# Performance work log

Hardware: AMD Instinct MI355X
Metric: run time of the kernel (lower is better)

Reference implementation:

```python
import jax, jax.numpy as jnp
import numpy as np
from jax import lax

B, CIN, COUT, H, W = 16, 128, 128, 128, 128
KH, KW = 3, 3
BLK_O, BLK_I = 32, 32          # block sizes over (out_ch, in_ch); kernel dims fully covered
PRUNING_RATE = 0.75


def _make_block_mask():
    # Reproduces blocksparse(): keep (1 - pruning_rate) of the channel blocks.
    nbo, nbi = COUT // BLK_O, CIN // BLK_I
    n_blocks = nbo * nbi
    n_keep = int(round(n_blocks * (1.0 - PRUNING_RATE)))
    rng = np.random.default_rng(42)
    keep = np.zeros(n_blocks, dtype=np.float32)
    keep[rng.permutation(n_blocks)[:n_keep]] = 1.0
    blk = keep.reshape(nbo, nbi)                     # [4, 4]
    m = np.kron(blk, np.ones((BLK_O, BLK_I), np.float32))   # [COUT, CIN]
    m = np.broadcast_to(m[:, :, None, None], (COUT, CIN, KH, KW))
    return jnp.asarray(np.ascontiguousarray(m))


def setup_inputs() -> dict:
    key = jax.random.key(0)
    k1, k2, k3 = jax.random.split(key, 3)
    x = jax.random.normal(k1, (B, CIN, H, W), dtype=jnp.float32)
    weight = jax.random.normal(k2, (COUT, CIN, KH, KW), dtype=jnp.float32) * 0.05
    bias = jax.random.normal(k3, (COUT,), dtype=jnp.float32) * 0.05
    mask = _make_block_mask()
    return {"x": x, "weight": weight, "bias": bias, "mask": mask}


def reference(x, weight, bias, mask):
    # weight = weight * mask, then standard dense conv2d (stride 1, pad 1, dil 1, groups 1)
    w = weight * mask
    y = lax.conv_general_dilated(
        x, w,
        window_strides=(1, 1),
        padding=((1, 1), (1, 1)),
        dimension_numbers=("NCHW", "OIHW", "NCHW"),
    )
    return y + bias[None, :, None, None]
```

## Files before the change

### kernel.cpp

```cpp
#include <hip/hip_runtime.h>

#define NBATCH 16
#define CIN_ 128
#define COUT_ 128
#define H_ 128
#define W_ 128
#define TH 4
#define NR (TH + 2)
#define PSTRIDE 32

typedef short bf16x8 __attribute__((ext_vector_type(8)));
typedef float f32x4 __attribute__((ext_vector_type(4)));
typedef unsigned short u16x8 __attribute__((ext_vector_type(8)));

__device__ __forceinline__ unsigned short f32_to_bf16(float f) {
  unsigned int u = __float_as_uint(f);
  u += 0x7fffu + ((u >> 16) & 1u);
  return (unsigned short)(u >> 16);
}

__global__ void make_lists_k(const float* __restrict__ mask, int* __restrict__ lists) {
  if (threadIdx.x == 0) {
    for (int i = 0; i < 20; ++i) lists[i] = 0;
    for (int ob = 0; ob < 4; ++ob) {
      int c = 0;
      for (int ib = 0; ib < 4; ++ib) {
        float v = mask[(size_t)((ob * 32) * CIN_ + ib * 32) * 9];
        if (v != 0.0f) { lists[4 + ob * 4 + c] = ib; ++c; }
      }
      lists[ob] = c;
    }
  }
}

__global__ __launch_bounds__(256) void pack_w_k(const float* __restrict__ weight,
                                                const float* __restrict__ mask,
                                                const int* __restrict__ lists,
                                                unsigned short* __restrict__ wpack) {
  const int khkw = blockIdx.x;
  const int slot = blockIdx.y;
  const int ob   = blockIdx.z;
  if (slot >= lists[ob]) return;
  const int ib = lists[4 + ob * 4 + slot];
  const int kh = khkw / 3, kw = khkw % 3;
  for (int e = threadIdx.x; e < 1024; e += 256) {
    const int co = e >> 5, ci = e & 31;
    const int cog = ob * 32 + co, cig = ib * 32 + ci;
    const size_t widx = ((size_t)(cog * CIN_ + cig) * 3 + kh) * 3 + kw;
    const float v = weight[widx] * mask[widx];
    wpack[(size_t)((ob * 4 + slot) * 9 + khkw) * 1024 + e] = f32_to_bf16(v);
  }
}

__global__ __launch_bounds__(256, 3) void conv_fused_k(const float* __restrict__ x,
                                                       const unsigned short* __restrict__ wpack,
                                                       const int* __restrict__ lists,
                                                       const float* __restrict__ bias,
                                                       float* __restrict__ out) {
  __shared__ unsigned short xs[NR * 130 * PSTRIDE];

  const int tid  = threadIdx.x;
  const int wave = tid >> 6;
  const int lane = tid & 63;
  const int wl   = lane & 15;
  const int kg   = lane >> 4;

  const int h0 = blockIdx.x * TH;
  const int b  = blockIdx.y;
  const int ob = blockIdx.z;
  const int w0 = wave * 32;

  const int cnt = lists[ob];

  f32x4 acc[TH][2][2] = {};

  const int g   = tid & 7;
  const int q   = tid >> 3;
  const int oct = g & 3;

  for (int s = 0; s < cnt; ++s) {
    const int ib = lists[4 + ob * 4 + s];

    if (s) __syncthreads();

    {
      const float* xbase =
          x + ((size_t)b * CIN_ + ib * 32 + oct * 8) * H_ * W_ + q * 4;
#pragma unroll
      for (int it = 0; it < 3; ++it) {
        const int r = it * 2 + (g >> 2);
        const int row = h0 - 1 + r;
        const bool rv = (row >= 0) && (row < H_);
        const float* src = xbase + (size_t)(rv ? row : 0) * W_;
        f32x4 v0 = *(const f32x4*)(src);
        f32x4 v1 = *(const f32x4*)(src + 1 * (size_t)H_ * W_);
        f32x4 v2 = *(const f32x4*)(src + 2 * (size_t)H_ * W_);
        f32x4 v3 = *(const f32x4*)(src + 3 * (size_t)H_ * W_);
        f32x4 v4 = *(const f32x4*)(src + 4 * (size_t)H_ * W_);
        f32x4 v5 = *(const f32x4*)(src + 5 * (size_t)H_ * W_);
        f32x4 v6 = *(const f32x4*)(src + 6 * (size_t)H_ * W_);
        f32x4 v7 = *(const f32x4*)(src + 7 * (size_t)H_ * W_);
#pragma unroll
        for (int j = 0; j < 4; ++j) {
          u16x8 o;
          if (rv) {
            o[0] = f32_to_bf16(v0[j]); o[1] = f32_to_bf16(v1[j]);
            o[2] = f32_to_bf16(v2[j]); o[3] = f32_to_bf16(v3[j]);
            o[4] = f32_to_bf16(v4[j]); o[5] = f32_to_bf16(v5[j]);
            o[6] = f32_to_bf16(v6[j]); o[7] = f32_to_bf16(v7[j]);
          } else {
            o = u16x8{0, 0, 0, 0, 0, 0, 0, 0};
          }
          *(u16x8*)(xs + (r * 130 + q * 4 + 1 + j) * PSTRIDE + oct * 8) = o;
        }
      }
      for (int e = tid; e < NR * 2 * 32; e += 256) {
        const int r = e >> 6, edge = (e >> 5) & 1, cc = e & 31;
        xs[(r * 130 + (edge ? 129 : 0)) * PSTRIDE + cc] = 0;
      }
    }

    const unsigned short* wk =
        wpack + (size_t)((ob * 4 + s) * 9) * 1024 + wl * 32 + kg * 8;
    bf16x8 a[3][3][2];
#pragma unroll
    for (int kh = 0; kh < 3; ++kh)
#pragma unroll
      for (int kw = 0; kw < 3; ++kw) {
        a[kh][kw][0] = *(const bf16x8*)(wk + (kh * 3 + kw) * 1024);
        a[kh][kw][1] = *(const bf16x8*)(wk + (kh * 3 + kw) * 1024 + 16 * 32);
      }

    __syncthreads();

#pragma unroll
    for (int ridx = 0; ridx < NR; ++ridx) {
      bf16x8 bf[2][3];
#pragma unroll
      for (int ni = 0; ni < 2; ++ni)
#pragma unroll
        for (int kw = 0; kw < 3; ++kw)
          bf[ni][kw] = *(const bf16x8*)(xs + (ridx * 130 + w0 + ni * 16 + wl + kw) * PSTRIDE + kg * 8);

#pragma unroll
      for (int kh = 0; kh < 3; ++kh) {
        const int hi = ridx - kh;
        if (hi < 0 || hi >= TH) continue;
#pragma unroll
        for (int kw = 0; kw < 3; ++kw) {
          acc[hi][0][0] = __builtin_amdgcn_mfma_f32_16x16x32_bf16(a[kh][kw][0], bf[0][kw], acc[hi][0][0], 0, 0, 0);
          acc[hi][0][1] = __builtin_amdgcn_mfma_f32_16x16x32_bf16(a[kh][kw][0], bf[1][kw], acc[hi][0][1], 0, 0, 0);
          acc[hi][1][0] = __builtin_amdgcn_mfma_f32_16x16x32_bf16(a[kh][kw][1], bf[0][kw], acc[hi][1][0], 0, 0, 0);
          acc[hi][1][1] = __builtin_amdgcn_mfma_f32_16x16x32_bf16(a[kh][kw][1], bf[1][kw], acc[hi][1][1], 0, 0, 0);
        }
      }
    }
  }

#pragma unroll
  for (int mi = 0; mi < 2; ++mi)
#pragma unroll
    for (int j = 0; j < 4; ++j) {
      const int co = mi * 16 + kg * 4 + j;
      const float bv = bias[ob * 32 + co];
#pragma unroll
      for (int hh = 0; hh < TH; ++hh) {
        float* yrow = out + ((size_t)(b * COUT_ + ob * 32 + co) * H_ + h0 + hh) * W_;
        yrow[w0 + wl]      = acc[hh][mi][0][j] + bv;
        yrow[w0 + wl + 16] = acc[hh][mi][1][j] + bv;
      }
    }
}

extern "C" void kernel_launch(void* const* d_in, const int* in_sizes, int n_in,
                              void* d_out, int out_size, void* d_ws, size_t ws_size,
                              hipStream_t stream) {
  const float* x      = (const float*)d_in[0];
  const float* weight = (const float*)d_in[1];
  const float* bias   = (const float*)d_in[2];
  const float* mask   = (const float*)d_in[3];
  float* out = (float*)d_out;

  int* lists = (int*)d_ws;
  unsigned short* wpack = (unsigned short*)((char*)d_ws + 4096);

  make_lists_k<<<1, 64, 0, stream>>>(mask, lists);
  pack_w_k<<<dim3(9, 4, 4), 256, 0, stream>>>(weight, mask, lists, wpack);
  conv_fused_k<<<dim3(H_ / TH, NBATCH, 4), 256, 0, stream>>>(x, wpack, lists, bias, out);
}
```

Measured before the change: 79.63 us.

## Drop list kernel, swizzle LDS input tile, stage output through LDS for vector stores

Removes the single-thread list-building kernel and instead has each block derive the kept input-channel blocks from the mask with a wave ballot and bit tricks, saving one launch. Applies an XOR swizzle to the LDS pixel layout to reduce bank conflicts on the MFMA operand reads. Rewrites the epilogue to stage accumulators through LDS so each lane writes contiguous 16-byte float4 stores instead of scattered scalar stores, adding a barrier and extra LDS traffic.

```diff
diff --git a/kernel.cpp b/kernel.cpp
--- a/kernel.cpp
+++ b/kernel.cpp
@@ -19,29 +19,27 @@
   return (unsigned short)(u >> 16);
 }
 
-__global__ void make_lists_k(const float* __restrict__ mask, int* __restrict__ lists) {
-  if (threadIdx.x == 0) {
-    for (int i = 0; i < 20; ++i) lists[i] = 0;
-    for (int ob = 0; ob < 4; ++ob) {
-      int c = 0;
-      for (int ib = 0; ib < 4; ++ib) {
-        float v = mask[(size_t)((ob * 32) * CIN_ + ib * 32) * 9];
-        if (v != 0.0f) { lists[4 + ob * 4 + c] = ib; ++c; }
-      }
-      lists[ob] = c;
-    }
-  }
+__device__ __forceinline__ int lx(int pix, int hw) {
+  return (pix * PSTRIDE + hw) ^ (((pix >> 2) & 1) << 5);
+}
+
+__device__ __forceinline__ int mask_bits(const float* __restrict__ mask, int ob, int lane) {
+  float mv = (lane < 4) ? mask[((size_t)(ob * 32) * CIN_ + lane * 32) * 9] : 0.0f;
+  unsigned long long bal = __ballot(mv != 0.0f);
+  return (int)(bal & 15ull);
 }
 
 __global__ __launch_bounds__(256) void pack_w_k(const float* __restrict__ weight,
                                                 const float* __restrict__ mask,
-                                                const int* __restrict__ lists,
                                                 unsigned short* __restrict__ wpack) {
   const int khkw = blockIdx.x;
   const int slot = blockIdx.y;
   const int ob   = blockIdx.z;
-  if (slot >= lists[ob]) return;
-  const int ib = lists[4 + ob * 4 + slot];
+  const int mb = mask_bits(mask, ob, threadIdx.x & 63);
+  if (slot >= __popc(mb)) return;
+  int m = mb;
+  for (int t = 0; t < slot; ++t) m &= m - 1;
+  const int ib = __ffs(m) - 1;
   const int kh = khkw / 3, kw = khkw % 3;
   for (int e = threadIdx.x; e < 1024; e += 256) {
     const int co = e >> 5, ci = e & 31;
@@ -54,10 +52,10 @@
 
 __global__ __launch_bounds__(256, 3) void conv_fused_k(const float* __restrict__ x,
                                                        const unsigned short* __restrict__ wpack,
-                                                       const int* __restrict__ lists,
+                                                       const float* __restrict__ mask,
                                                        const float* __restrict__ bias,
                                                        float* __restrict__ out) {
-  __shared__ unsigned short xs[NR * 130 * PSTRIDE];
+  __shared__ __align__(16) unsigned short xs[NR * 130 * PSTRIDE];
 
   const int tid  = threadIdx.x;
   const int wave = tid >> 6;
@@ -70,7 +68,8 @@
   const int ob = blockIdx.z;
   const int w0 = wave * 32;
 
-  const int cnt = lists[ob];
+  const int mb  = mask_bits(mask, ob, lane);
+  const int cnt = __popc(mb);
 
   f32x4 acc[TH][2][2] = {};
 
@@ -78,8 +77,10 @@
   const int q   = tid >> 3;
   const int oct = g & 3;
 
+  int mrem = mb;
   for (int s = 0; s < cnt; ++s) {
-    const int ib = lists[4 + ob * 4 + s];
+    const int ib = __ffs(mrem) - 1;
+    mrem &= mrem - 1;
 
     if (s) __syncthreads();
 
@@ -111,12 +112,12 @@
           } else {
             o = u16x8{0, 0, 0, 0, 0, 0, 0, 0};
           }
-          *(u16x8*)(xs + (r * 130 + q * 4 + 1 + j) * PSTRIDE + oct * 8) = o;
+          *(u16x8*)(xs + lx(r * 130 + q * 4 + 1 + j, oct * 8)) = o;
         }
       }
       for (int e = tid; e < NR * 2 * 32; e += 256) {
         const int r = e >> 6, edge = (e >> 5) & 1, cc = e & 31;
-        xs[(r * 130 + (edge ? 129 : 0)) * PSTRIDE + cc] = 0;
+        xs[lx(r * 130 + (edge ? 129 : 0), cc)] = 0;
       }
     }
 
@@ -140,7 +141,7 @@
       for (int ni = 0; ni < 2; ++ni)
 #pragma unroll
         for (int kw = 0; kw < 3; ++kw)
-          bf[ni][kw] = *(const bf16x8*)(xs + (ridx * 130 + w0 + ni * 16 + wl + kw) * PSTRIDE + kg * 8);
+          bf[ni][kw] = *(const bf16x8*)(xs + lx(ridx * 130 + w0 + ni * 16 + wl + kw, kg * 8));
 
 #pragma unroll
       for (int kh = 0; kh < 3; ++kh) {
@@ -157,19 +158,39 @@
     }
   }
 
-#pragma unroll
-  for (int mi = 0; mi < 2; ++mi)
-#pragma unroll
-    for (int j = 0; j < 4; ++j) {
-      const int co = mi * 16 + kg * 4 + j;
-      const float bv = bias[ob * 32 + co];
-#pragma unroll
-      for (int hh = 0; hh < TH; ++hh) {
-        float* yrow = out + ((size_t)(b * COUT_ + ob * 32 + co) * H_ + h0 + hh) * W_;
-        yrow[w0 + wl]      = acc[hh][mi][0][j] + bv;
-        yrow[w0 + wl + 16] = acc[hh][mi][1][j] + bv;
-      }
-    }
+  __syncthreads();
+  float* scr = (float*)xs;
+  const int seg = lane & 7;
+  const int cq  = lane >> 3;
+#pragma unroll
+  for (int p = 0; p < 2; ++p) {
+#pragma unroll
+    for (int e = 0; e < 2; ++e) {
+      const int hh = p * 2 + e;
+      float* sb = scr + (wave * 2 + e) * 1152;
+#pragma unroll
+      for (int mi = 0; mi < 2; ++mi)
+#pragma unroll
+        for (int j = 0; j < 4; ++j) {
+          const int co = mi * 16 + kg * 4 + j;
+          const float bv = bias[ob * 32 + co];
+          sb[co * 36 + wl]      = acc[hh][mi][0][j] + bv;
+          sb[co * 36 + 16 + wl] = acc[hh][mi][1][j] + bv;
+        }
+    }
+#pragma unroll
+    for (int e = 0; e < 2; ++e) {
+      const int hh = p * 2 + e;
+      const float* sb = scr + (wave * 2 + e) * 1152;
+#pragma unroll
+      for (int c2 = 0; c2 < 4; ++c2) {
+        const int co = c2 * 8 + cq;
+        f32x4 v = *(const f32x4*)(sb + co * 36 + seg * 4);
+        *(f32x4*)(out + ((size_t)(b * COUT_ + ob * 32 + co) * H_ + h0 + hh) * W_ +
+                  w0 + seg * 4) = v;
+      }
+    }
+  }
 }
 
 extern "C" void kernel_launch(void* const* d_in, const int* in_sizes, int n_in,
@@ -181,10 +202,8 @@
   const float* mask   = (const float*)d_in[3];
   float* out = (float*)d_out;
 
-  int* lists = (int*)d_ws;
-  unsigned short* wpack = (unsigned short*)((char*)d_ws + 4096);
-
-  make_lists_k<<<1, 64, 0, stream>>>(mask, lists);
-  pack_w_k<<<dim3(9, 4, 4), 256, 0, stream>>>(weight, mask, lists, wpack);
-  conv_fused_k<<<dim3(H_ / TH, NBATCH, 4), 256, 0, stream>>>(x, wpack, lists, bias, out);
-}
+  unsigned short* wpack = (unsigned short*)d_ws;
+
+  pack_w_k<<<dim3(9, 4, 4), 256, 0, stream>>>(weight, mask, wpack);
+  conv_fused_k<<<dim3(H_ / TH, NBATCH, 4), 256, 0, stream>>>(x, wpack, mask, bias, out);
+}
```

Result: slower. 114.5 us (+43.8%).
